# Kernel optimization log

Hardware: AMD Instinct MI355X
Metric: run time of the kernel (lower is better)

## Reference

```python
import jax, jax.numpy as jnp
import numpy as np

HIDDEN = 2048
NUM_HEADS = 16
Q_LORA = 1536
KV_LORA = 512
QK_NOPE = 128
QK_ROPE = 64
V_HEAD = 128
EPS = 1e-6
QK_HEAD = QK_NOPE + QK_ROPE  # 192


def rmsnorm(x, w, eps=EPS):
    xf = x.astype(jnp.float32)
    var = jnp.mean(xf * xf, axis=-1, keepdims=True)
    return (w * (xf * jax.lax.rsqrt(var + eps)).astype(x.dtype))


def setup_inputs() -> dict:
    key = jax.random.key(0)
    ks = jax.random.split(key, 8)
    B, S = 1, 2048
    hidden_states = jax.random.normal(ks[0], (B, S, HIDDEN), dtype=jnp.float32)
    # causal additive mask [B,1,S,S]
    causal = jnp.tril(jnp.ones((S, S), dtype=bool))
    attention_mask = jnp.where(causal, 0.0, -1e9).astype(jnp.float32)[None, None]
    s = lambda fan_in: 1.0 / np.sqrt(fan_in)
    Wqa = jax.random.normal(ks[1], (HIDDEN, Q_LORA), dtype=jnp.float32) * s(HIDDEN)
    gqa = jnp.ones((Q_LORA,), dtype=jnp.float32)
    Wqb = jax.random.normal(ks[2], (Q_LORA, NUM_HEADS * QK_HEAD), dtype=jnp.float32) * s(Q_LORA)
    Wkva = jax.random.normal(ks[3], (HIDDEN, KV_LORA + QK_ROPE), dtype=jnp.float32) * s(HIDDEN)
    gkva = jnp.ones((KV_LORA,), dtype=jnp.float32)
    Wkvb = jax.random.normal(ks[4], (KV_LORA, NUM_HEADS * (QK_NOPE + V_HEAD)), dtype=jnp.float32) * s(KV_LORA)
    Wo = jax.random.normal(ks[5], (NUM_HEADS * V_HEAD, HIDDEN), dtype=jnp.float32) * s(NUM_HEADS * V_HEAD)
    return {"hidden_states": hidden_states, "attention_mask": attention_mask,
            "Wqa": Wqa, "gqa": gqa, "Wqb": Wqb, "Wkva": Wkva, "gkva": gkva,
            "Wkvb": Wkvb, "Wo": Wo}


def reference(hidden_states, attention_mask, Wqa, gqa, Wqb, Wkva, gkva, Wkvb, Wo):
    B, S, _ = hidden_states.shape
    # Q path: low-rank down-proj + RMSNorm + up-proj
    q_c = rmsnorm(hidden_states @ Wqa, gqa)
    q = (q_c @ Wqb).reshape(B, S, NUM_HEADS, QK_HEAD).transpose(0, 2, 1, 3)  # [B,H,S,192]
    # KV path: joint down-proj, split latent and shared rope part
    kv_c = hidden_states @ Wkva  # [B,S,KV_LORA+ROPE]
    kv_a, k_rope = kv_c[..., :KV_LORA], kv_c[..., KV_LORA:]
    kv = (rmsnorm(kv_a, gkva) @ Wkvb).reshape(B, S, NUM_HEADS, QK_NOPE + V_HEAD)
    k_nope, v = kv[..., :QK_NOPE], kv[..., QK_NOPE:]
    # shared rope part broadcast across heads (no rotary actually applied in source)
    k_rope_b = jnp.broadcast_to(k_rope[:, :, None, :], (B, S, NUM_HEADS, QK_ROPE))
    k = jnp.concatenate([k_nope, k_rope_b], axis=-1).transpose(0, 2, 1, 3)  # [B,H,S,192]
    v = v.transpose(0, 2, 1, 3)  # [B,H,S,128]
    scale = 1.0 / np.sqrt(QK_HEAD)
    attn = jnp.einsum("bhqd,bhkd->bhqk", q, k) * scale
    attn = attn + attention_mask
    attn = jax.nn.softmax(attn.astype(jnp.float32), axis=-1).astype(v.dtype)
    out = jnp.einsum("bhqk,bhkd->bhqd", attn, v)  # [B,H,S,128]
    out = out.transpose(0, 2, 1, 3).reshape(B, S, NUM_HEADS * V_HEAD)
    return out @ Wo
```

## Files before the change

kernel.cpp:

```cpp
#include <hip/hip_runtime.h>
#include <hip/hip_bf16.h>

typedef __bf16 bf16;
typedef __bf16 bf16x8 __attribute__((ext_vector_type(8)));
typedef __bf16 bf16x4 __attribute__((ext_vector_type(4)));
typedef float f32x4 __attribute__((ext_vector_type(4)));

#define HIDDEN 2048
#define SEQ 2048
#define NH 16
#define QL 1536
#define KVL 512
#define SCALE_LOG2E 0.10411754631f

__device__ __forceinline__ void gload_lds16(const void* g, void* l) {
  typedef const __attribute__((address_space(1))) void* gp_t;
  typedef __attribute__((address_space(3))) void* lp_t;
  __builtin_amdgcn_global_load_lds((gp_t)(unsigned long long)g,
                                   (lp_t)(unsigned int)(unsigned long long)l, 16, 0, 0);
}

__device__ __forceinline__ float fexp2(float x) {
  float r; asm("v_exp_f32 %0, %1" : "=v"(r) : "v"(x)); return r;
}
__device__ __forceinline__ unsigned cvt_pk_bf16(float lo, float hi) {
  unsigned r; asm("v_cvt_pk_bf16_f32 %0, %1, %2" : "=v"(r) : "v"(lo), "v"(hi)); return r;
}

__global__ void k_prep(const float* __restrict__ hidden, bf16* __restrict__ Xb,
                       const float* __restrict__ Wqa, bf16* __restrict__ WqaT,
                       const float* __restrict__ Wqb, bf16* __restrict__ WqbT,
                       const float* __restrict__ Wkva, bf16* __restrict__ WkvaT,
                       const float* __restrict__ Wkvb, bf16* __restrict__ WkvbT,
                       const float* __restrict__ Wo, bf16* __restrict__ WoT) {
  __shared__ float tile[32][33];
  int b = blockIdx.x, tid = threadIdx.x;
  const float* W; bf16* Wt; int K, N, bx, by;
  if (b < 3072)       { W = Wqa;  Wt = WqaT;  K = 2048; N = 1536; int r = b;         bx = r % 48;  by = r / 48; }
  else if (b < 7680)  { W = Wqb;  Wt = WqbT;  K = 1536; N = 3072; int r = b - 3072;  bx = r % 96;  by = r / 96; }
  else if (b < 8832)  { W = Wkva; Wt = WkvaT; K = 2048; N = 576;  int r = b - 7680;  bx = r % 18;  by = r / 18; }
  else if (b < 10880) { W = Wkvb; Wt = WkvbT; K = 512;  N = 4096; int r = b - 8832;  bx = r % 128; by = r / 128; }
  else if (b < 14976) { W = Wo;   Wt = WoT;   K = 2048; N = 2048; int r = b - 10880; bx = r % 64;  by = r / 64; }
  else {
    int r = b - 14976;
    int base = (r * 256 + tid) * 4;
    float4 v = *(const float4*)(hidden + base);
    bf16x4 o = { (bf16)v.x, (bf16)v.y, (bf16)v.z, (bf16)v.w };
    *(bf16x4*)(Xb + base) = o;
    return;
  }
  int n0 = bx * 32, k0 = by * 32, cc = tid & 31, rr = tid >> 5;
#pragma unroll
  for (int it = 0; it < 4; ++it) {
    int r = it * 8 + rr;
    tile[r][cc] = W[(size_t)(k0 + r) * N + n0 + cc];
  }
  __syncthreads();
#pragma unroll
  for (int it = 0; it < 4; ++it) {
    int r = it * 8 + rr;
    Wt[(size_t)(n0 + r) * K + k0 + cc] = (bf16)tile[cc][r];
  }
}

__device__ __forceinline__ void gemm_epilogue(f32x4 acc[4][4], bf16* Cb, float* Cf,
                                              int N, int m0, int n0, bf16* VTout) {
  int lane = threadIdx.x & 63, w = threadIdx.x >> 6;
  int wr = w >> 1, wc = w & 1;
  int l15 = lane & 15, l4 = lane >> 4;
#pragma unroll
  for (int m = 0; m < 4; ++m)
#pragma unroll
    for (int n = 0; n < 4; ++n)
#pragma unroll
      for (int r = 0; r < 4; ++r) {
        int grow = m0 + wr * 64 + m * 16 + l4 * 4 + r;
        int gcol = n0 + wc * 64 + n * 16 + l15;
        if (gcol < N) {
          float v = acc[m][n][r];
          if (Cf) Cf[(size_t)grow * N + gcol] = v;
          else Cb[(size_t)grow * N + gcol] = (bf16)v;
          if (VTout && (gcol & 255) >= 128) {
            int d = (gcol >> 8) * 128 + (gcol & 255) - 128;
            VTout[(size_t)d * 2048 + grow] = (bf16)v;
          }
        }
      }
}

__device__ __forceinline__ void gemm_body(const bf16* __restrict__ A, const bf16* __restrict__ Bt,
                                          bf16* __restrict__ Cb, float* __restrict__ Cf,
                                          int N, int Kfull, int kbase, int Klen,
                                          int m0, int n0, bf16* As, bf16* Bs, bf16* VTout) {
  int tid = threadIdx.x, lane = tid & 63, w = tid >> 6;
  int wr = w >> 1, wc = w & 1;
  int l15 = lane & 15, l4 = lane >> 4;
  f32x4 acc[4][4] = {};
  for (int k0 = kbase; k0 < kbase + Klen; k0 += 64) {
#pragma unroll
    for (int i = 0; i < 4; ++i) {
      int c = w * 4 + i;
      int row = c * 8 + (lane >> 3);
      int col = (lane & 7) * 8;
      gload_lds16(&A[(size_t)(m0 + row) * Kfull + k0 + col], &As[c * 512]);
      gload_lds16(&Bt[(size_t)(n0 + row) * Kfull + k0 + col], &Bs[c * 512]);
    }
    __syncthreads();
#pragma unroll
    for (int kk = 0; kk < 2; ++kk) {
      bf16x8 af[4], bfr[4];
#pragma unroll
      for (int m = 0; m < 4; ++m)
        af[m] = *(const bf16x8*)&As[(wr * 64 + m * 16 + l15) * 64 + kk * 32 + l4 * 8];
#pragma unroll
      for (int n = 0; n < 4; ++n)
        bfr[n] = *(const bf16x8*)&Bs[(wc * 64 + n * 16 + l15) * 64 + kk * 32 + l4 * 8];
      __builtin_amdgcn_s_setprio(1);
#pragma unroll
      for (int m = 0; m < 4; ++m)
#pragma unroll
        for (int n = 0; n < 4; ++n)
          acc[m][n] = __builtin_amdgcn_mfma_f32_16x16x32_bf16(af[m], bfr[n], acc[m][n], 0, 0, 0);
      __builtin_amdgcn_s_setprio(0);
    }
    __syncthreads();
  }
  gemm_epilogue(acc, Cb, Cf, N, m0, n0, VTout);
}

__device__ __forceinline__ void gemm_body_pf(const bf16* __restrict__ A, const bf16* __restrict__ Bt,
                                             bf16* __restrict__ Cb, float* __restrict__ Cf,
                                             int N, int Kfull, int kbase, int Klen,
                                             int m0, int n0, bf16* AsD, bf16* BsD) {
  int tid = threadIdx.x, lane = tid & 63, w = tid >> 6;
  int wr = w >> 1, wc = w & 1;
  int l15 = lane & 15, l4 = lane >> 4;
  f32x4 acc[4][4] = {};

  auto STAGE = [&](int buf, int k0) {
#pragma unroll
    for (int i = 0; i < 4; ++i) {
      int c = w * 4 + i;
      int row = c * 8 + (lane >> 3);
      int col = (lane & 7) * 8;
      gload_lds16(&A[(size_t)(m0 + row) * Kfull + k0 + col], &AsD[buf * 8192 + c * 512]);
      gload_lds16(&Bt[(size_t)(n0 + row) * Kfull + k0 + col], &BsD[buf * 8192 + c * 512]);
    }
  };

  int nT = Klen >> 6;
  STAGE(0, kbase);
  for (int tt = 0; tt < nT; ++tt) {
    int cur = tt & 1;
    if (tt + 1 < nT) {
      STAGE(cur ^ 1, kbase + (tt + 1) * 64);
      asm volatile("s_waitcnt vmcnt(8)" ::: "memory");
    } else {
      asm volatile("s_waitcnt vmcnt(0)" ::: "memory");
    }
    __builtin_amdgcn_s_barrier();
    __builtin_amdgcn_sched_barrier(0);
    const bf16* As = &AsD[cur * 8192];
    const bf16* Bs = &BsD[cur * 8192];
#pragma unroll
    for (int kk = 0; kk < 2; ++kk) {
      bf16x8 af[4], bfr[4];
#pragma unroll
      for (int m = 0; m < 4; ++m)
        af[m] = *(const bf16x8*)&As[(wr * 64 + m * 16 + l15) * 64 + kk * 32 + l4 * 8];
#pragma unroll
      for (int n = 0; n < 4; ++n)
        bfr[n] = *(const bf16x8*)&Bs[(wc * 64 + n * 16 + l15) * 64 + kk * 32 + l4 * 8];
      __builtin_amdgcn_s_setprio(1);
#pragma unroll
      for (int m = 0; m < 4; ++m)
#pragma unroll
        for (int n = 0; n < 4; ++n)
          acc[m][n] = __builtin_amdgcn_mfma_f32_16x16x32_bf16(af[m], bfr[n], acc[m][n], 0, 0, 0);
      __builtin_amdgcn_s_setprio(0);
    }
    __builtin_amdgcn_s_barrier();
  }
  gemm_epilogue(acc, Cb, Cf, N, m0, n0, nullptr);
}

__global__ __launch_bounds__(256) void k_gemm_a(const bf16* __restrict__ Xb,
                                                const bf16* __restrict__ B1, const bf16* __restrict__ B2,
                                                float* __restrict__ qa0, float* __restrict__ qa1,
                                                float* __restrict__ kvc0, float* __restrict__ kvc1) {
  __shared__ __align__(16) bf16 AsD[2 * 128 * 64];
  __shared__ __align__(16) bf16 BsD[2 * 128 * 64];
  int by = blockIdx.y;
  if (by < 24) {
    int yy = by >> 1, kh = by & 1;
    gemm_body_pf(Xb, B1, nullptr, kh ? qa1 : qa0, 1536, 2048, kh * 1024, 1024,
                 blockIdx.x * 128, yy * 128, AsD, BsD);
  } else {
    int r = by - 24, yy = r >> 1, kh = r & 1;
    gemm_body_pf(Xb, B2, nullptr, kh ? kvc1 : kvc0, 576, 2048, kh * 1024, 1024,
                 blockIdx.x * 128, yy * 128, AsD, BsD);
  }
}

__global__ __launch_bounds__(256) void k_gemm_b(const bf16* __restrict__ A1, const bf16* __restrict__ A2,
                                                const bf16* __restrict__ B1, const bf16* __restrict__ B2,
                                                bf16* __restrict__ C1, bf16* __restrict__ C2,
                                                bf16* __restrict__ VT) {
  __shared__ __align__(16) bf16 As[128 * 64];
  __shared__ __align__(16) bf16 Bs[128 * 64];
  int by = blockIdx.y;
  if (by < 24) gemm_body(A1, B1, C1, nullptr, 3072, 1536, 0, 1536, blockIdx.x * 128, by * 128, As, Bs, nullptr);
  else         gemm_body(A2, B2, C2, nullptr, 4096, 512, 0, 512, blockIdx.x * 128, (by - 24) * 128, As, Bs, VT);
}

__global__ __launch_bounds__(256) void k_gemm_sk(const bf16* __restrict__ A, const bf16* __restrict__ Bt,
                                                 float* __restrict__ O0, float* __restrict__ O1) {
  __shared__ __align__(16) bf16 AsD[2 * 128 * 64];
  __shared__ __align__(16) bf16 BsD[2 * 128 * 64];
  int by = blockIdx.y, nt = by >> 1, kh = by & 1;
  gemm_body_pf(A, Bt, nullptr, kh ? O1 : O0, 2048, 2048, kh * 1024, 1024,
               blockIdx.x * 128, nt * 128, AsD, BsD);
}

__global__ void k_add(const float* __restrict__ O0, const float* __restrict__ O1,
                      float* __restrict__ out) {
  int base = (blockIdx.x * 256 + threadIdx.x) * 4;
  float4 a = *(const float4*)(O0 + base);
  float4 b = *(const float4*)(O1 + base);
  float4 o = { a.x + b.x, a.y + b.y, a.z + b.z, a.w + b.w };
  *(float4*)(out + base) = o;
}

__device__ inline float block_reduce_sum(float v, float* red) {
#pragma unroll
  for (int off = 1; off < 64; off <<= 1) v += __shfl_xor(v, off);
  int w = threadIdx.x >> 6;
  if ((threadIdx.x & 63) == 0) red[w] = v;
  __syncthreads();
  return red[0] + red[1] + red[2] + red[3];
}

__global__ void k_rms_all(const float* __restrict__ qa0, const float* __restrict__ qa1,
                          const float* __restrict__ gq, bf16* __restrict__ qc,
                          const float* __restrict__ kvc0, const float* __restrict__ kvc1,
                          const float* __restrict__ gkv,
                          bf16* __restrict__ kvn, bf16* __restrict__ kr) {
  __shared__ float red[4];
  int b = blockIdx.x, tid = threadIdx.x;
  if (b < 2048) {
    int row = b;
    float v[6];
    float ss = 0.f;
#pragma unroll
    for (int j = 0; j < 6; ++j) {
      size_t idx = (size_t)row * QL + tid + j * 256;
      v[j] = qa0[idx] + qa1[idx];
      ss += v[j] * v[j];
    }
    float tot = block_reduce_sum(ss, red);
    float rs = rsqrtf(tot / (float)QL + 1e-6f);
#pragma unroll
    for (int j = 0; j < 6; ++j) {
      int c = tid + j * 256;
      qc[(size_t)row * QL + c] = (bf16)(v[j] * rs * gq[c]);
    }
  } else {
    int row = b - 2048;
    size_t base = (size_t)row * 576;
    float v0 = kvc0[base + tid] + kvc1[base + tid];
    float v1 = kvc0[base + tid + 256] + kvc1[base + tid + 256];
    float tot = block_reduce_sum(v0 * v0 + v1 * v1, red);
    float rs = rsqrtf(tot / (float)KVL + 1e-6f);
    kvn[(size_t)row * KVL + tid] = (bf16)(v0 * rs * gkv[tid]);
    kvn[(size_t)row * KVL + tid + 256] = (bf16)(v1 * rs * gkv[tid + 256]);
    if (tid < 64) kr[row * 64 + tid] = (bf16)(kvc0[base + 512 + tid] + kvc1[base + 512 + tid]);
  }
}

__global__ __launch_bounds__(256) void k_attn(const bf16* __restrict__ Q, const bf16* __restrict__ KV,
                                              const bf16* __restrict__ KR, const bf16* __restrict__ VT,
                                              bf16* __restrict__ O) {
  __shared__ __align__(16) bf16 KsD[2][64 * 192];
  __shared__ __align__(16) bf16 VtD[2][128 * 64];
  int bid = blockIdx.x;
  int h = bid & 15, i = bid >> 4;
  int qb = (i < 16) ? i : 47 - i;
  int q0 = qb * 64;
  int tid = threadIdx.x, lane = tid & 63, w = tid >> 6;
  int l15 = lane & 15, l4 = lane >> 4;
  int sw = (l15 & 7) << 4;
  const bf16* VTh = VT + (size_t)h * 128 * 2048;

  bf16x8 aq[6];
  int qrow = q0 + w * 16 + l15;
#pragma unroll
  for (int ks = 0; ks < 6; ++ks)
    aq[ks] = *(const bf16x8*)&Q[(size_t)qrow * 3072 + h * 192 + ks * 32 + l4 * 8];

  f32x4 oacc[8] = {};
  float mrun = -1e30f, lrun = 0.f;
  int nt = qb + 1;

  auto STAGE = [&](int buf, int t) {
    char* kb = (char*)KsD[buf];
    char* vb = (char*)VtD[buf];
#pragma unroll
    for (int it = 0; it < 6; ++it) {
      int idx = it * 256 + tid;
      int r = idx / 24, gg = idx - r * 24;
      int c = gg ^ (r & 7);
      const bf16* src = (c < 16) ? &KV[(size_t)(t * 64 + r) * 4096 + h * 256 + c * 8]
                                 : &KR[(size_t)(t * 64 + r) * 64 + (c - 16) * 8];
      gload_lds16(src, kb + (it * 256 + w * 64) * 16);
    }
#pragma unroll
    for (int it = 0; it < 4; ++it) {
      int idx = it * 256 + tid;
      int d = idx >> 3, c2 = idx & 7, c = c2 ^ (d & 7);
      gload_lds16(&VTh[(size_t)d * 2048 + t * 64 + c * 8], vb + (it * 256 + w * 64) * 16);
    }
  };

  STAGE(0, 0);
  for (int t = 0; t < nt; ++t) {
    int cur = t & 1;
    if (t + 1 < nt) {
      STAGE(cur ^ 1, t + 1);
      asm volatile("s_waitcnt vmcnt(10)" ::: "memory");
    } else {
      asm volatile("s_waitcnt vmcnt(0)" ::: "memory");
    }
    __builtin_amdgcn_s_barrier();
    __builtin_amdgcn_sched_barrier(0);
    const char* Kb = (const char*)KsD[cur];
    const char* Vb = (const char*)VtD[cur];

    f32x4 sacc[4] = {};
    __builtin_amdgcn_s_setprio(1);
#pragma unroll
    for (int ks = 0; ks < 6; ++ks) {
      int co = (((ks << 2) + l4) << 4) ^ sw;
#pragma unroll
      for (int n = 0; n < 4; ++n) {
        bf16x8 ak = *(const bf16x8*)(Kb + (n * 16 + l15) * 384 + co);
        sacc[n] = __builtin_amdgcn_mfma_f32_16x16x32_bf16(ak, aq[ks], sacc[n], 0, 0, 0);
      }
    }
    __builtin_amdgcn_s_setprio(0);

    bool maskt = (t == qb);
#pragma unroll
    for (int n = 0; n < 4; ++n)
#pragma unroll
      for (int r = 0; r < 4; ++r) {
        float v = sacc[n][r] * SCALE_LOG2E;
        if (maskt) {
          int kvp = t * 64 + n * 16 + l4 * 4 + r;
          if (kvp > qrow) v = -1e30f;
        }
        sacc[n][r] = v;
      }

    float mx = sacc[0][0];
#pragma unroll
    for (int n = 0; n < 4; ++n)
#pragma unroll
      for (int r = 0; r < 4; ++r) mx = fmaxf(mx, sacc[n][r]);
    mx = fmaxf(mx, __shfl_xor(mx, 16));
    mx = fmaxf(mx, __shfl_xor(mx, 32));
    if (__any(mx - mrun > 8.0f)) {
      float mn = fmaxf(mrun, mx);
      float al = fexp2(mrun - mn);
      mrun = mn;
      lrun *= al;
#pragma unroll
      for (int vf = 0; vf < 8; ++vf) oacc[vf] *= al;
    }
    float rsum = 0.f;
    unsigned pk[4][2];
#pragma unroll
    for (int n = 0; n < 4; ++n) {
      float e0 = fexp2(sacc[n][0] - mrun);
      float e1 = fexp2(sacc[n][1] - mrun);
      float e2 = fexp2(sacc[n][2] - mrun);
      float e3 = fexp2(sacc[n][3] - mrun);
      rsum += (e0 + e1) + (e2 + e3);
      pk[n][0] = cvt_pk_bf16(e0, e1);
      pk[n][1] = cvt_pk_bf16(e2, e3);
    }
    rsum += __shfl_xor(rsum, 16);
    rsum += __shfl_xor(rsum, 32);
    lrun += rsum;

    int srcA = l15 + ((l4 & 1) << 5);
    int srcB = srcA + 16;
    int sel = l4 >> 1;
    __builtin_amdgcn_s_setprio(1);
#pragma unroll
    for (int ks = 0; ks < 2; ++ks) {
      unsigned a00 = (unsigned)__shfl((int)pk[2 * ks][0], srcA);
      unsigned a10 = (unsigned)__shfl((int)pk[2 * ks + 1][0], srcA);
      unsigned a01 = (unsigned)__shfl((int)pk[2 * ks][1], srcA);
      unsigned a11 = (unsigned)__shfl((int)pk[2 * ks + 1][1], srcA);
      unsigned b00 = (unsigned)__shfl((int)pk[2 * ks][0], srcB);
      unsigned b10 = (unsigned)__shfl((int)pk[2 * ks + 1][0], srcB);
      unsigned b01 = (unsigned)__shfl((int)pk[2 * ks][1], srcB);
      unsigned b11 = (unsigned)__shfl((int)pk[2 * ks + 1][1], srcB);
      union { unsigned u[4]; bf16x8 v; } ap;
      ap.u[0] = sel ? a10 : a00;
      ap.u[1] = sel ? a11 : a01;
      ap.u[2] = sel ? b10 : b00;
      ap.u[3] = sel ? b11 : b01;
      int co = (((ks << 2) + l4) << 4) ^ sw;
#pragma unroll
      for (int vf = 0; vf < 8; ++vf) {
        bf16x8 av = *(const bf16x8*)(Vb + (vf * 16 + l15) * 128 + co);
        oacc[vf] = __builtin_amdgcn_mfma_f32_16x16x32_bf16(av, ap.v, oacc[vf], 0, 0, 0);
      }
    }
    __builtin_amdgcn_s_setprio(0);
    __builtin_amdgcn_s_barrier();
  }

  int curF = (nt - 1) & 1;
  char* OTw = (char*)KsD[curF] + w * 4096;
  float inv = 1.0f / lrun;
#pragma unroll
  for (int vf = 0; vf < 8; ++vf) {
    unsigned ua = cvt_pk_bf16(oacc[vf][0] * inv, oacc[vf][1] * inv);
    unsigned ub = cvt_pk_bf16(oacc[vf][2] * inv, oacc[vf][3] * inv);
    int base = vf * 32 + l4 * 8;
    *(unsigned*)(OTw + l15 * 256 + ((base + 0) ^ sw)) = ua;
    *(unsigned*)(OTw + l15 * 256 + ((base + 4) ^ sw)) = ub;
  }
  int qq = lane >> 2, c0 = lane & 3;
  size_t obase = (size_t)(q0 + w * 16 + qq) * 2048 + h * 128;
#pragma unroll
  for (int ii = 0; ii < 4; ++ii) {
    int ck = ii * 4 + c0;
    bf16x8 v = *(const bf16x8*)(OTw + qq * 256 + ((ck * 16) ^ ((qq & 7) << 4)));
    *(bf16x8*)&O[obase + ck * 8] = v;
  }
}

extern "C" void kernel_launch(void* const* d_in, const int* in_sizes, int n_in,
                              void* d_out, int out_size, void* d_ws, size_t ws_size,
                              hipStream_t stream) {
  (void)in_sizes; (void)n_in; (void)out_size; (void)ws_size;
  const float* hidden = (const float*)d_in[0];
  const float* Wqa  = (const float*)d_in[2];
  const float* gqa  = (const float*)d_in[3];
  const float* Wqb  = (const float*)d_in[4];
  const float* Wkva = (const float*)d_in[5];
  const float* gkva = (const float*)d_in[6];
  const float* Wkvb = (const float*)d_in[7];
  const float* Wo   = (const float*)d_in[8];
  float* out = (float*)d_out;

  char* ws = (char*)d_ws;
  size_t off = 0;
  auto alloc = [&](size_t bytes) {
    char* p = ws + off;
    off += (bytes + 255) & ~(size_t)255;
    return p;
  };
  bf16* Xb     = (bf16*)alloc((size_t)SEQ * HIDDEN * 2);
  bf16* WqaT   = (bf16*)alloc((size_t)QL * HIDDEN * 2);
  bf16* WqbT   = (bf16*)alloc((size_t)3072 * QL * 2);
  bf16* WkvaT  = (bf16*)alloc((size_t)576 * HIDDEN * 2);
  bf16* WkvbT  = (bf16*)alloc((size_t)4096 * KVL * 2);
  bf16* WoT    = (bf16*)alloc((size_t)2048 * 2048 * 2);
  float* qa0   = (float*)alloc((size_t)SEQ * QL * 4);
  float* qa1   = (float*)alloc((size_t)SEQ * QL * 4);
  float* kvc0  = (float*)alloc((size_t)SEQ * 576 * 4);
  float* kvc1  = (float*)alloc((size_t)SEQ * 576 * 4);
  bf16* qc     = (bf16*)alloc((size_t)SEQ * QL * 2);
  bf16* kvn    = (bf16*)alloc((size_t)SEQ * KVL * 2);
  bf16* krope  = (bf16*)alloc((size_t)SEQ * 64 * 2);
  bf16* Qm     = (bf16*)alloc((size_t)SEQ * 3072 * 2);
  bf16* KVm    = (bf16*)alloc((size_t)SEQ * 4096 * 2);
  bf16* VTg    = (bf16*)alloc((size_t)NH * 128 * SEQ * 2);
  bf16* Om     = (bf16*)alloc((size_t)SEQ * 2048 * 2);
  float* O0 = qa0;
  float* O1 = (float*)KVm;

  k_prep<<<19072, 256, 0, stream>>>(hidden, Xb, Wqa, WqaT, Wqb, WqbT,
                                    Wkva, WkvaT, Wkvb, WkvbT, Wo, WoT);
  k_gemm_a<<<dim3(16, 34), 256, 0, stream>>>(Xb, WqaT, WkvaT, qa0, qa1, kvc0, kvc1);
  k_rms_all<<<4096, 256, 0, stream>>>(qa0, qa1, gqa, qc, kvc0, kvc1, gkva, kvn, krope);
  k_gemm_b<<<dim3(16, 56), 256, 0, stream>>>(qc, kvn, WqbT, WkvbT, Qm, KVm, VTg);
  k_attn<<<512, 256, 0, stream>>>(Qm, KVm, krope, VTg, Om);
  k_gemm_sk<<<dim3(16, 32), 256, 0, stream>>>(Om, WoT, O0, O1);
  k_add<<<4096, 256, 0, stream>>>(O0, O1, out);
}
```

Before: 205.7 us.

## Split attention over KV ranges with 128-row Q tiles and a combine kernel

After: 215.1 us. 4.6% more time.

```diff
diff --git a/kernel.cpp b/kernel.cpp
--- a/kernel.cpp
+++ b/kernel.cpp
@@ -26,6 +26,8 @@
 __device__ __forceinline__ unsigned cvt_pk_bf16(float lo, float hi) {
   unsigned r; asm("v_cvt_pk_bf16_f32 %0, %1, %2" : "=v"(r) : "v"(lo), "v"(hi)); return r;
 }
+
+union pkvec { unsigned u[4]; bf16x8 v; };
 
 __global__ void k_prep(const float* __restrict__ hidden, bf16* __restrict__ Xb,
                        const float* __restrict__ Wqa, bf16* __restrict__ WqaT,
@@ -279,27 +281,30 @@
 
 __global__ __launch_bounds__(256) void k_attn(const bf16* __restrict__ Q, const bf16* __restrict__ KV,
                                               const bf16* __restrict__ KR, const bf16* __restrict__ VT,
-                                              bf16* __restrict__ O) {
+                                              bf16* __restrict__ Opart, float2* __restrict__ Ml) {
   __shared__ __align__(16) bf16 KsD[2][64 * 192];
   __shared__ __align__(16) bf16 VtD[2][128 * 64];
   int bid = blockIdx.x;
-  int h = bid & 15, i = bid >> 4;
-  int qb = (i < 16) ? i : 47 - i;
-  int q0 = qb * 64;
+  int h = bid & 15, s = bid >> 4;
+  int qbp, t0, t1;
+  if (s < 16) { qbp = s;      t0 = 0;        t1 = qbp + 1; }
+  else        { qbp = 31 - s; t0 = qbp + 1;  t1 = 2 * qbp + 2; }
+  int q0 = qbp * 128;
   int tid = threadIdx.x, lane = tid & 63, w = tid >> 6;
   int l15 = lane & 15, l4 = lane >> 4;
   int sw = (l15 & 7) << 4;
   const bf16* VTh = VT + (size_t)h * 128 * 2048;
 
-  bf16x8 aq[6];
-  int qrow = q0 + w * 16 + l15;
-#pragma unroll
-  for (int ks = 0; ks < 6; ++ks)
-    aq[ks] = *(const bf16x8*)&Q[(size_t)qrow * 3072 + h * 192 + ks * 32 + l4 * 8];
-
-  f32x4 oacc[8] = {};
-  float mrun = -1e30f, lrun = 0.f;
-  int nt = qb + 1;
+  bf16x8 aq0[6], aq1[6];
+  int qrow0 = q0 + w * 32 + l15;
+#pragma unroll
+  for (int ks = 0; ks < 6; ++ks) {
+    aq0[ks] = *(const bf16x8*)&Q[(size_t)qrow0 * 3072 + h * 192 + ks * 32 + l4 * 8];
+    aq1[ks] = *(const bf16x8*)&Q[(size_t)(qrow0 + 16) * 3072 + h * 192 + ks * 32 + l4 * 8];
+  }
+
+  f32x4 oacc0[8] = {}, oacc1[8] = {};
+  float mrun0 = -1e30f, mrun1 = -1e30f, lrun0 = 0.f, lrun1 = 0.f;
 
   auto STAGE = [&](int buf, int t) {
     char* kb = (char*)KsD[buf];
@@ -321,10 +326,10 @@
     }
   };
 
-  STAGE(0, 0);
-  for (int t = 0; t < nt; ++t) {
-    int cur = t & 1;
-    if (t + 1 < nt) {
+  STAGE(0, t0);
+  for (int t = t0; t < t1; ++t) {
+    int cur = (t - t0) & 1;
+    if (t + 1 < t1) {
       STAGE(cur ^ 1, t + 1);
       asm volatile("s_waitcnt vmcnt(10)" ::: "memory");
     } else {
@@ -335,7 +340,10 @@
     const char* Kb = (const char*)KsD[cur];
     const char* Vb = (const char*)VtD[cur];
 
-    f32x4 sacc[4] = {};
+    bool maskt = (t >= 2 * qbp);
+    unsigned pk0[4][2], pk1[4][2];
+
+    f32x4 s0[4] = {}, s1[4] = {};
     __builtin_amdgcn_s_setprio(1);
 #pragma unroll
     for (int ks = 0; ks < 6; ++ks) {
@@ -343,54 +351,98 @@
 #pragma unroll
       for (int n = 0; n < 4; ++n) {
         bf16x8 ak = *(const bf16x8*)(Kb + (n * 16 + l15) * 384 + co);
-        sacc[n] = __builtin_amdgcn_mfma_f32_16x16x32_bf16(ak, aq[ks], sacc[n], 0, 0, 0);
+        s0[n] = __builtin_amdgcn_mfma_f32_16x16x32_bf16(ak, aq0[ks], s0[n], 0, 0, 0);
+        s1[n] = __builtin_amdgcn_mfma_f32_16x16x32_bf16(ak, aq1[ks], s1[n], 0, 0, 0);
       }
     }
     __builtin_amdgcn_s_setprio(0);
 
-    bool maskt = (t == qb);
-#pragma unroll
-    for (int n = 0; n < 4; ++n)
-#pragma unroll
-      for (int r = 0; r < 4; ++r) {
-        float v = sacc[n][r] * SCALE_LOG2E;
-        if (maskt) {
-          int kvp = t * 64 + n * 16 + l4 * 4 + r;
-          if (kvp > qrow) v = -1e30f;
+    {
+      int qrow = qrow0;
+#pragma unroll
+      for (int n = 0; n < 4; ++n)
+#pragma unroll
+        for (int r = 0; r < 4; ++r) {
+          float v = s0[n][r] * SCALE_LOG2E;
+          if (maskt) {
+            int kvp = t * 64 + n * 16 + l4 * 4 + r;
+            if (kvp > qrow) v = -1e30f;
+          }
+          s0[n][r] = v;
         }
-        sacc[n][r] = v;
-      }
-
-    float mx = sacc[0][0];
-#pragma unroll
-    for (int n = 0; n < 4; ++n)
-#pragma unroll
-      for (int r = 0; r < 4; ++r) mx = fmaxf(mx, sacc[n][r]);
-    mx = fmaxf(mx, __shfl_xor(mx, 16));
-    mx = fmaxf(mx, __shfl_xor(mx, 32));
-    if (__any(mx - mrun > 8.0f)) {
-      float mn = fmaxf(mrun, mx);
-      float al = fexp2(mrun - mn);
-      mrun = mn;
-      lrun *= al;
-#pragma unroll
-      for (int vf = 0; vf < 8; ++vf) oacc[vf] *= al;
-    }
-    float rsum = 0.f;
-    unsigned pk[4][2];
-#pragma unroll
-    for (int n = 0; n < 4; ++n) {
-      float e0 = fexp2(sacc[n][0] - mrun);
-      float e1 = fexp2(sacc[n][1] - mrun);
-      float e2 = fexp2(sacc[n][2] - mrun);
-      float e3 = fexp2(sacc[n][3] - mrun);
-      rsum += (e0 + e1) + (e2 + e3);
-      pk[n][0] = cvt_pk_bf16(e0, e1);
-      pk[n][1] = cvt_pk_bf16(e2, e3);
-    }
-    rsum += __shfl_xor(rsum, 16);
-    rsum += __shfl_xor(rsum, 32);
-    lrun += rsum;
+      float mx = s0[0][0];
+#pragma unroll
+      for (int n = 0; n < 4; ++n)
+#pragma unroll
+        for (int r = 0; r < 4; ++r) mx = fmaxf(mx, s0[n][r]);
+      mx = fmaxf(mx, __shfl_xor(mx, 16));
+      mx = fmaxf(mx, __shfl_xor(mx, 32));
+      if (__any(mx - mrun0 > 8.0f)) {
+        float mn = fmaxf(mrun0, mx);
+        float al = fexp2(mrun0 - mn);
+        mrun0 = mn;
+        lrun0 *= al;
+#pragma unroll
+        for (int vf = 0; vf < 8; ++vf) oacc0[vf] *= al;
+      }
+      float rsum = 0.f;
+#pragma unroll
+      for (int n = 0; n < 4; ++n) {
+        float e0 = fexp2(s0[n][0] - mrun0);
+        float e1 = fexp2(s0[n][1] - mrun0);
+        float e2 = fexp2(s0[n][2] - mrun0);
+        float e3 = fexp2(s0[n][3] - mrun0);
+        rsum += (e0 + e1) + (e2 + e3);
+        pk0[n][0] = cvt_pk_bf16(e0, e1);
+        pk0[n][1] = cvt_pk_bf16(e2, e3);
+      }
+      rsum += __shfl_xor(rsum, 16);
+      rsum += __shfl_xor(rsum, 32);
+      lrun0 += rsum;
+    }
+    {
+      int qrow = qrow0 + 16;
+#pragma unroll
+      for (int n = 0; n < 4; ++n)
+#pragma unroll
+        for (int r = 0; r < 4; ++r) {
+          float v = s1[n][r] * SCALE_LOG2E;
+          if (maskt) {
+            int kvp = t * 64 + n * 16 + l4 * 4 + r;
+            if (kvp > qrow) v = -1e30f;
+          }
+          s1[n][r] = v;
+        }
+      float mx = s1[0][0];
+#pragma unroll
+      for (int n = 0; n < 4; ++n)
+#pragma unroll
+        for (int r = 0; r < 4; ++r) mx = fmaxf(mx, s1[n][r]);
+      mx = fmaxf(mx, __shfl_xor(mx, 16));
+      mx = fmaxf(mx, __shfl_xor(mx, 32));
+      if (__any(mx - mrun1 > 8.0f)) {
+        float mn = fmaxf(mrun1, mx);
+        float al = fexp2(mrun1 - mn);
+        mrun1 = mn;
+        lrun1 *= al;
+#pragma unroll
+        for (int vf = 0; vf < 8; ++vf) oacc1[vf] *= al;
+      }
+      float rsum = 0.f;
+#pragma unroll
+      for (int n = 0; n < 4; ++n) {
+        float e0 = fexp2(s1[n][0] - mrun1);
+        float e1 = fexp2(s1[n][1] - mrun1);
+        float e2 = fexp2(s1[n][2] - mrun1);
+        float e3 = fexp2(s1[n][3] - mrun1);
+        rsum += (e0 + e1) + (e2 + e3);
+        pk1[n][0] = cvt_pk_bf16(e0, e1);
+        pk1[n][1] = cvt_pk_bf16(e2, e3);
+      }
+      rsum += __shfl_xor(rsum, 16);
+      rsum += __shfl_xor(rsum, 32);
+      lrun1 += rsum;
+    }
 
     int srcA = l15 + ((l4 & 1) << 5);
     int srcB = srcA + 16;
@@ -398,48 +450,98 @@
     __builtin_amdgcn_s_setprio(1);
 #pragma unroll
     for (int ks = 0; ks < 2; ++ks) {
-      unsigned a00 = (unsigned)__shfl((int)pk[2 * ks][0], srcA);
-      unsigned a10 = (unsigned)__shfl((int)pk[2 * ks + 1][0], srcA);
-      unsigned a01 = (unsigned)__shfl((int)pk[2 * ks][1], srcA);
-      unsigned a11 = (unsigned)__shfl((int)pk[2 * ks + 1][1], srcA);
-      unsigned b00 = (unsigned)__shfl((int)pk[2 * ks][0], srcB);
-      unsigned b10 = (unsigned)__shfl((int)pk[2 * ks + 1][0], srcB);
-      unsigned b01 = (unsigned)__shfl((int)pk[2 * ks][1], srcB);
-      unsigned b11 = (unsigned)__shfl((int)pk[2 * ks + 1][1], srcB);
-      union { unsigned u[4]; bf16x8 v; } ap;
-      ap.u[0] = sel ? a10 : a00;
-      ap.u[1] = sel ? a11 : a01;
-      ap.u[2] = sel ? b10 : b00;
-      ap.u[3] = sel ? b11 : b01;
+      pkvec ap0, ap1;
+      {
+        unsigned a0 = (unsigned)__shfl((int)pk0[2 * ks][0], srcA);
+        unsigned a1 = (unsigned)__shfl((int)pk0[2 * ks + 1][0], srcA);
+        unsigned a2 = (unsigned)__shfl((int)pk0[2 * ks][1], srcA);
+        unsigned a3 = (unsigned)__shfl((int)pk0[2 * ks + 1][1], srcA);
+        unsigned b0 = (unsigned)__shfl((int)pk0[2 * ks][0], srcB);
+        unsigned b1 = (unsigned)__shfl((int)pk0[2 * ks + 1][0], srcB);
+        unsigned b2 = (unsigned)__shfl((int)pk0[2 * ks][1], srcB);
+        unsigned b3 = (unsigned)__shfl((int)pk0[2 * ks + 1][1], srcB);
+        ap0.u[0] = sel ? a1 : a0;
+        ap0.u[1] = sel ? a3 : a2;
+        ap0.u[2] = sel ? b1 : b0;
+        ap0.u[3] = sel ? b3 : b2;
+      }
+      {
+        unsigned a0 = (unsigned)__shfl((int)pk1[2 * ks][0], srcA);
+        unsigned a1 = (unsigned)__shfl((int)pk1[2 * ks + 1][0], srcA);
+        unsigned a2 = (unsigned)__shfl((int)pk1[2 * ks][1], srcA);
+        unsigned a3 = (unsigned)__shfl((int)pk1[2 * ks + 1][1], srcA);
+        unsigned b0 = (unsigned)__shfl((int)pk1[2 * ks][0], srcB);
+        unsigned b1 = (unsigned)__shfl((int)pk1[2 * ks + 1][0], srcB);
+        unsigned b2 = (unsigned)__shfl((int)pk1[2 * ks][1], srcB);
+        unsigned b3 = (unsigned)__shfl((int)pk1[2 * ks + 1][1], srcB);
+        ap1.u[0] = sel ? a1 : a0;
+        ap1.u[1] = sel ? a3 : a2;
+        ap1.u[2] = sel ? b1 : b0;
+        ap1.u[3] = sel ? b3 : b2;
+      }
       int co = (((ks << 2) + l4) << 4) ^ sw;
 #pragma unroll
       for (int vf = 0; vf < 8; ++vf) {
         bf16x8 av = *(const bf16x8*)(Vb + (vf * 16 + l15) * 128 + co);
-        oacc[vf] = __builtin_amdgcn_mfma_f32_16x16x32_bf16(av, ap.v, oacc[vf], 0, 0, 0);
+        oacc0[vf] = __builtin_amdgcn_mfma_f32_16x16x32_bf16(av, ap0.v, oacc0[vf], 0, 0, 0);
+        oacc1[vf] = __builtin_amdgcn_mfma_f32_16x16x32_bf16(av, ap1.v, oacc1[vf], 0, 0, 0);
       }
     }
     __builtin_amdgcn_s_setprio(0);
     __builtin_amdgcn_s_barrier();
   }
 
-  int curF = (nt - 1) & 1;
+  int curF = (t1 - 1 - t0) & 1;
   char* OTw = (char*)KsD[curF] + w * 4096;
-  float inv = 1.0f / lrun;
-#pragma unroll
-  for (int vf = 0; vf < 8; ++vf) {
-    unsigned ua = cvt_pk_bf16(oacc[vf][0] * inv, oacc[vf][1] * inv);
-    unsigned ub = cvt_pk_bf16(oacc[vf][2] * inv, oacc[vf][3] * inv);
-    int base = vf * 32 + l4 * 8;
-    *(unsigned*)(OTw + l15 * 256 + ((base + 0) ^ sw)) = ua;
-    *(unsigned*)(OTw + l15 * 256 + ((base + 4) ^ sw)) = ub;
-  }
+  bf16* Op = Opart + (size_t)bid * 128 * 128;
   int qq = lane >> 2, c0 = lane & 3;
-  size_t obase = (size_t)(q0 + w * 16 + qq) * 2048 + h * 128;
-#pragma unroll
-  for (int ii = 0; ii < 4; ++ii) {
-    int ck = ii * 4 + c0;
-    bf16x8 v = *(const bf16x8*)(OTw + qq * 256 + ((ck * 16) ^ ((qq & 7) << 4)));
-    *(bf16x8*)&O[obase + ck * 8] = v;
+#pragma unroll
+  for (int g = 0; g < 2; ++g) {
+    const f32x4* oa = g ? oacc1 : oacc0;
+#pragma unroll
+    for (int vf = 0; vf < 8; ++vf) {
+      unsigned ua = cvt_pk_bf16(oa[vf][0], oa[vf][1]);
+      unsigned ub = cvt_pk_bf16(oa[vf][2], oa[vf][3]);
+      int base = vf * 32 + l4 * 8;
+      *(unsigned*)(OTw + l15 * 256 + ((base + 0) ^ sw)) = ua;
+      *(unsigned*)(OTw + l15 * 256 + ((base + 4) ^ sw)) = ub;
+    }
+    int row = w * 32 + g * 16 + qq;
+#pragma unroll
+    for (int ii = 0; ii < 4; ++ii) {
+      int ck = ii * 4 + c0;
+      bf16x8 v = *(const bf16x8*)(OTw + qq * 256 + ((ck * 16) ^ ((qq & 7) << 4)));
+      *(bf16x8*)&Op[(size_t)row * 128 + ck * 8] = v;
+    }
+    if (l4 == 0)
+      Ml[(size_t)bid * 128 + w * 32 + g * 16 + l15] =
+          make_float2(g ? mrun1 : mrun0, g ? lrun1 : lrun0);
+  }
+}
+
+__global__ __launch_bounds__(256) void k_comb(const bf16* __restrict__ Opart,
+                                              const float2* __restrict__ Ml,
+                                              bf16* __restrict__ O) {
+  int b = blockIdx.x, h = b & 15, qbp = b >> 4;
+  int bidA = qbp * 16 + h, bidB = (31 - qbp) * 16 + h;
+  int tid = threadIdx.x;
+  int rr = tid >> 5, col = (tid & 31) * 4;
+#pragma unroll
+  for (int rp = 0; rp < 16; ++rp) {
+    int row = rp * 8 + rr;
+    float2 mlA = Ml[(size_t)bidA * 128 + row];
+    float2 mlB = Ml[(size_t)bidB * 128 + row];
+    float M = fmaxf(mlA.x, mlB.x);
+    float wA = fexp2(mlA.x - M), wB = fexp2(mlB.x - M);
+    float L = wA * mlA.y + wB * mlB.y;
+    float inv = 1.0f / L;
+    bf16x4 vA = *(const bf16x4*)&Opart[(size_t)bidA * 16384 + row * 128 + col];
+    bf16x4 vB = *(const bf16x4*)&Opart[(size_t)bidB * 16384 + row * 128 + col];
+    bf16x4 o;
+#pragma unroll
+    for (int j = 0; j < 4; ++j)
+      o[j] = (bf16)((wA * (float)vA[j] + wB * (float)vB[j]) * inv);
+    *(bf16x4*)&O[(size_t)(qbp * 128 + row) * 2048 + h * 128 + col] = o;
   }
 }
 
@@ -481,6 +583,8 @@
   bf16* KVm    = (bf16*)alloc((size_t)SEQ * 4096 * 2);
   bf16* VTg    = (bf16*)alloc((size_t)NH * 128 * SEQ * 2);
   bf16* Om     = (bf16*)alloc((size_t)SEQ * 2048 * 2);
+  float2* Ml   = (float2*)alloc((size_t)512 * 128 * 8);
+  bf16* Opart  = (bf16*)qa0;
   float* O0 = qa0;
   float* O1 = (float*)KVm;
 
@@ -489,7 +593,8 @@
   k_gemm_a<<<dim3(16, 34), 256, 0, stream>>>(Xb, WqaT, WkvaT, qa0, qa1, kvc0, kvc1);
   k_rms_all<<<4096, 256, 0, stream>>>(qa0, qa1, gqa, qc, kvc0, kvc1, gkva, kvn, krope);
   k_gemm_b<<<dim3(16, 56), 256, 0, stream>>>(qc, kvn, WqbT, WkvbT, Qm, KVm, VTg);
-  k_attn<<<512, 256, 0, stream>>>(Qm, KVm, krope, VTg, Om);
+  k_attn<<<512, 256, 0, stream>>>(Qm, KVm, krope, VTg, Opart, Ml);
+  k_comb<<<256, 256, 0, stream>>>(Opart, Ml, Om);
   k_gemm_sk<<<dim3(16, 32), 256, 0, stream>>>(Om, WoT, O0, O1);
   k_add<<<4096, 256, 0, stream>>>(O0, O1, out);
 }
```
